# Optimization experiments

Hardware: AMD Instinct MI355X
Metric: run time of the kernel (lower is better)

The kernel has to match this reference:

```python
import jax, jax.numpy as jnp
import numpy as np

B, L, D = 4, 2048, 1024


def setup_inputs() -> dict:
    key = jax.random.key(0)
    ks = jax.random.split(key, 7)
    scale = 1.0 / np.sqrt(D)
    x = jax.random.normal(ks[0], (B, L, D), dtype=jnp.float32)
    wq = jax.random.normal(ks[1], (D, D), dtype=jnp.float32) * scale
    wk = jax.random.normal(ks[2], (D, D), dtype=jnp.float32) * scale
    wv = jax.random.normal(ks[3], (D, D), dtype=jnp.float32) * scale
    bq = jnp.zeros((D,), dtype=jnp.float32)
    bk = jnp.zeros((D,), dtype=jnp.float32)
    bv = jnp.zeros((D,), dtype=jnp.float32)
    # causal decoder mask, shape [B, 1, L, L] as produced by nn.make_causal_mask
    causal = jnp.tril(jnp.ones((L, L), dtype=bool))
    mask = jnp.broadcast_to(causal[None, None, :, :], (B, 1, L, L))
    return {"x": x, "mask": mask, "wq": wq, "bq": bq, "wk": wk, "bk": bk, "wv": wv, "bv": bv}


def reference(x, mask, wq, bq, wk, bk, wv, bv):
    # q/k/v projections (Dense with bias)
    q = x @ wq + bq            # [B, L, D]
    k = x @ wk + bk
    v = x @ wv + bv
    depth = q.shape[-1]
    q = q / jnp.sqrt(jnp.asarray(depth, dtype=q.dtype))
    attn = jnp.einsum('bqd,bkd->bqk', q, k)          # [B, L, L]
    attn = jnp.where(jnp.squeeze(mask), attn, -999999)
    attn = jax.nn.softmax(attn, axis=-1)
    out = attn @ v                                    # [B, L, D]
    return out
```

## Files before the change

kernel.cpp:

```cpp
#include <hip/hip_runtime.h>

typedef __bf16 bf16_t;
typedef __attribute__((ext_vector_type(8))) __bf16 bf16x8;
typedef __attribute__((ext_vector_type(4))) __bf16 bf16x4;
typedef __attribute__((ext_vector_type(4))) float f32x4;

#define B_  4
#define L_  2048
#define D_  1024
#define M_  (B_*L_)
#define N3_ (3*D_)

__device__ __forceinline__ void gload_lds16(const void* g, void* l) {
  __builtin_amdgcn_global_load_lds(
      (__attribute__((address_space(1))) void*)(g),
      (__attribute__((address_space(3))) void*)(l), 16, 0, 0);
}

__device__ __forceinline__ void stage_half(const bf16_t* __restrict__ g, int ld, int grow0,
                                           int k0, bf16_t* lds_tile, int h, int tid) {
  const int lane = tid & 63;
  const int csrc = ((lane & 7) ^ (lane >> 3)) << 3;
  const int rsub = tid >> 3;
  bf16_t* l0 = lds_tile + (size_t)(h * 128 + ((tid >> 6) << 3)) * 64;
  const bf16_t* g0 = g + (size_t)(grow0 + h * 128 + rsub) * ld + (k0 + csrc);
  gload_lds16(g0, l0);
  gload_lds16(g0 + (size_t)64 * ld, l0 + 64 * 64);
}

__global__ __launch_bounds__(512, 2)
void gemm256(const bf16_t* __restrict__ A, int lda,
             const bf16_t* __restrict__ Bt, int ldb,
             bf16_t* __restrict__ C, int ldc,
             const float* __restrict__ b0, const float* __restrict__ b1,
             const float* __restrict__ b2, int K)
{
  const int gx = gridDim.x;
  const int nwg = gx * gridDim.y;
  const int orig = blockIdx.y * gx + blockIdx.x;
  const int swz = (orig & 7) * (nwg >> 3) + (orig >> 3);
  const int bx = swz % gx, by = swz / gx;

  const int r0 = by * 256, c0 = bx * 256;
  const int NT = K >> 6;

  extern __shared__ __align__(16) bf16_t smem[];
  bf16_t* A0 = smem;
  bf16_t* A1 = smem + 16384;
  bf16_t* A2 = smem + 32768;
  bf16_t* B0 = smem + 49152;
  bf16_t* B1 = smem + 65536;

  const int tid = threadIdx.x;
  const int wid = tid >> 6, lane = tid & 63;
  const int wm = wid >> 2, wn = wid & 3;
  const int rl = lane & 15, cg = lane >> 4, x0 = lane & 7;
  const int co0 = ((cg ^ x0) << 3);
  const int co1 = (((4 + cg) ^ x0) << 3);
  const int aoff = (wm * 128 + rl) * 64;
  const int boff = (wn * 64 + rl) * 64;

  f32x4 acc[8][4] = {};
  bf16x8 aLo_[4][2], aHi_[4][2], bF[4][2];

  stage_half(A,  lda, r0, 0,  A0, 0, tid);  stage_half(A,  lda, r0, 0,  A0, 1, tid);
  stage_half(Bt, ldb, c0, 0,  B0, 0, tid);  stage_half(Bt, ldb, c0, 0,  B0, 1, tid);
  stage_half(A,  lda, r0, 64, A1, 0, tid);  stage_half(A,  lda, r0, 64, A1, 1, tid);
  stage_half(Bt, ldb, c0, 64, B1, 0, tid);  stage_half(Bt, ldb, c0, 64, B1, 1, tid);
  asm volatile("s_waitcnt vmcnt(8)" ::: "memory");
  asm volatile("s_barrier" ::: "memory");
  #pragma unroll
  for (int mi = 0; mi < 4; ++mi) {
    aLo_[mi][0] = *(const bf16x8*)(A0 + aoff + mi * 1024 + co0);
    aLo_[mi][1] = *(const bf16x8*)(A0 + aoff + mi * 1024 + co1);
  }

  for (int j = 0; j < NT; ++j) {
    #pragma unroll
    for (int ni = 0; ni < 4; ++ni) {
      bF[ni][0] = *(const bf16x8*)(B0 + boff + ni * 1024 + co0);
      bF[ni][1] = *(const bf16x8*)(B0 + boff + ni * 1024 + co1);
    }
    #pragma unroll
    for (int mi = 0; mi < 4; ++mi) {
      aHi_[mi][0] = *(const bf16x8*)(A0 + aoff + (4 + mi) * 1024 + co0);
      aHi_[mi][1] = *(const bf16x8*)(A0 + aoff + (4 + mi) * 1024 + co1);
    }
    if (j + 2 < NT) {
      stage_half(A, lda, r0, (j + 2) * 64, A2, 0, tid);
      stage_half(A, lda, r0, (j + 2) * 64, A2, 1, tid);
    }
    asm volatile("s_waitcnt lgkmcnt(0)" ::: "memory");
    __builtin_amdgcn_sched_barrier(0);
    __builtin_amdgcn_s_setprio(1);
    #pragma unroll
    for (int mi = 0; mi < 4; ++mi)
      #pragma unroll
      for (int ni = 0; ni < 4; ++ni) {
        acc[mi][ni] = __builtin_amdgcn_mfma_f32_16x16x32_bf16(
            bF[ni][0], aLo_[mi][0], acc[mi][ni], 0, 0, 0);
        acc[mi][ni] = __builtin_amdgcn_mfma_f32_16x16x32_bf16(
            bF[ni][1], aLo_[mi][1], acc[mi][ni], 0, 0, 0);
      }
    __builtin_amdgcn_s_setprio(0);
    if (j + 2 < NT) asm volatile("s_waitcnt vmcnt(4)" ::: "memory");
    else            asm volatile("s_waitcnt vmcnt(0)" ::: "memory");
    asm volatile("s_barrier" ::: "memory");

    if (j + 1 < NT) {
      #pragma unroll
      for (int mi = 0; mi < 4; ++mi) {
        aLo_[mi][0] = *(const bf16x8*)(A1 + aoff + mi * 1024 + co0);
        aLo_[mi][1] = *(const bf16x8*)(A1 + aoff + mi * 1024 + co1);
      }
      if (j + 2 < NT) {
        stage_half(Bt, ldb, c0, (j + 2) * 64, B0, 0, tid);
        stage_half(Bt, ldb, c0, (j + 2) * 64, B0, 1, tid);
      }
      asm volatile("s_waitcnt lgkmcnt(8)" ::: "memory");
    } else {
      asm volatile("s_waitcnt lgkmcnt(0)" ::: "memory");
    }
    __builtin_amdgcn_sched_barrier(0);
    __builtin_amdgcn_s_setprio(1);
    #pragma unroll
    for (int mi = 0; mi < 4; ++mi)
      #pragma unroll
      for (int ni = 0; ni < 4; ++ni) {
        acc[4 + mi][ni] = __builtin_amdgcn_mfma_f32_16x16x32_bf16(
            bF[ni][0], aHi_[mi][0], acc[4 + mi][ni], 0, 0, 0);
        acc[4 + mi][ni] = __builtin_amdgcn_mfma_f32_16x16x32_bf16(
            bF[ni][1], aHi_[mi][1], acc[4 + mi][ni], 0, 0, 0);
      }
    __builtin_amdgcn_s_setprio(0);
    asm volatile("s_barrier" ::: "memory");

    bf16_t* t = A0; A0 = A1; A1 = A2; A2 = t;
    t = B0; B0 = B1; B1 = t;
  }

  const int ng = cg * 4;
  #pragma unroll
  for (int mi = 0; mi < 8; ++mi) {
    const int r = r0 + wm * 128 + mi * 16 + rl;
    #pragma unroll
    for (int ni = 0; ni < 4; ++ni) {
      const int c = c0 + wn * 64 + ni * 16 + ng;
      const float* bias = (c < D_) ? b0 : (c < 2 * D_) ? b1 : b2;
      const float4 bb = *(const float4*)(bias + (c & (D_ - 1)));
      const float sc = (c < D_) ? 0.03125f : 1.0f;
      f32x4 v = acc[mi][ni];
      bf16x4 o = {(bf16_t)((v[0] + bb.x) * sc), (bf16_t)((v[1] + bb.y) * sc),
                  (bf16_t)((v[2] + bb.z) * sc), (bf16_t)((v[3] + bb.w) * sc)};
      *(bf16x4*)(C + (size_t)r * ldc + c) = o;
    }
  }
}

#define KTILE(J, AC, AN1, AN2, BCr, BNx, bC, bN)                                  \
  do {                                                                            \
    const int j_ = (J);                                                           \
    _Pragma("unroll")                                                             \
    for (int mi = 0; mi < 4; ++mi) {                                              \
      aM1_[mi][0] = *(const bf16x8*)(AC + abase + (4 + mi) * 2048 + co0);         \
      aM1_[mi][1] = *(const bf16x8*)(AC + abase + (4 + mi) * 2048 + co1);         \
    }                                                                             \
    if (j_ + 2 < NT) {                                                            \
      stage_half(A, lda, r0, (j_ + 2) * 64, AN2, 0, tid);                         \
      stage_half(A, lda, r0, (j_ + 2) * 64, AN2, 1, tid);                         \
    }                                                                             \
    asm volatile("s_waitcnt lgkmcnt(8)" ::: "memory");                            \
    __builtin_amdgcn_sched_barrier(0);                                            \
    __builtin_amdgcn_s_setprio(1);                                                \
    _Pragma("unroll")                                                             \
    for (int mi = 0; mi < 4; ++mi)                                                \
      _Pragma("unroll")                                                           \
      for (int ni = 0; ni < 2; ++ni) {                                            \
        acc[mi][ni] = __builtin_amdgcn_mfma_f32_16x16x32_bf16(                    \
            bC[ni][0], aM0_[mi][0], acc[mi][ni], 0, 0, 0);                        \
        acc[mi][ni] = __builtin_amdgcn_mfma_f32_16x16x32_bf16(                    \
            bC[ni][1], aM0_[mi][1], acc[mi][ni], 0, 0, 0);                        \
      }                                                                           \
    __builtin_amdgcn_s_setprio(0);                                                \
    if (j_ + 2 < NT) asm volatile("s_waitcnt vmcnt(4)" ::: "memory");             \
    else             asm volatile("s_waitcnt vmcnt(0)" ::: "memory");             \
    asm volatile("s_barrier" ::: "memory");                                       \
    if (j_ + 1 < NT) {                                                            \
      _Pragma("unroll")                                                           \
      for (int mi = 0; mi < 4; ++mi) {                                            \
        aM0_[mi][0] = *(const bf16x8*)(AN1 + abase + mi * 2048 + co0);            \
        aM0_[mi][1] = *(const bf16x8*)(AN1 + abase + mi * 2048 + co1);            \
      }                                                                           \
      _Pragma("unroll")                                                           \
      for (int ni = 0; ni < 2; ++ni) {                                            \
        bN[ni][0] = *(const bf16x8*)(BNx + bbase + ni * 1024 + co0);              \
        bN[ni][1] = *(const bf16x8*)(BNx + bbase + ni * 1024 + co1);              \
      }                                                                           \
      if (j_ + 2 < NT)                                                            \
        stage_half(Bt, ldb, c0, (j_ + 2) * 64, BCr, 0, tid);                      \
      asm volatile("s_waitcnt lgkmcnt(12)" ::: "memory");                         \
    } else {                                                                      \
      asm volatile("s_waitcnt lgkmcnt(0)" ::: "memory");                          \
    }                                                                             \
    __builtin_amdgcn_sched_barrier(0);                                            \
    __builtin_amdgcn_s_setprio(1);                                                \
    _Pragma("unroll")                                                             \
    for (int mi = 0; mi < 4; ++mi)                                                \
      _Pragma("unroll")                                                           \
      for (int ni = 0; ni < 2; ++ni) {                                            \
        acc[4 + mi][ni] = __builtin_amdgcn_mfma_f32_16x16x32_bf16(                \
            bC[ni][0], aM1_[mi][0], acc[4 + mi][ni], 0, 0, 0);                    \
        acc[4 + mi][ni] = __builtin_amdgcn_mfma_f32_16x16x32_bf16(                \
            bC[ni][1], aM1_[mi][1], acc[4 + mi][ni], 0, 0, 0);                    \
      }                                                                           \
    __builtin_amdgcn_s_setprio(0);                                                \
    asm volatile("s_barrier" ::: "memory");                                       \
  } while (0)

template<bool OUT_BF16, bool CAUSAL, bool VARK>
__global__ __launch_bounds__(512, 2)
void gemm8(const bf16_t* __restrict__ A, int lda, long sA,
           const bf16_t* __restrict__ Bt, int ldb, long sB,
           void* __restrict__ Cv, int ldc, long sC, int K)
{
  const int gx = gridDim.x;
  const int nwg = gx * gridDim.y;
  const int orig = blockIdx.y * gx + blockIdx.x;
  const int swz = (orig & 7) * (nwg >> 3) + (orig >> 3);
  const int bx = swz % gx, by = swz / gx;
  if (CAUSAL && bx > 2 * by + 1) return;

  const int z = blockIdx.z;
  A  += (size_t)z * sA;
  Bt += (size_t)z * sB;

  const int r0 = by * 256, c0 = bx * 128;
  const int kend = VARK ? min(K, r0 + 256) : K;
  const int NT = kend >> 6;

  extern __shared__ __align__(16) bf16_t smem[];
  bf16_t* Ab0 = smem;
  bf16_t* Ab1 = smem + 16384;
  bf16_t* Ab2 = smem + 32768;
  bf16_t* Bb0 = smem + 49152;
  bf16_t* Bb1 = smem + 57344;

  const int tid = threadIdx.x;
  const int wid = tid >> 6, lane = tid & 63;
  const int wm = wid >> 2, wn = wid & 3;
  const int rl = lane & 15, cg = lane >> 4, x0 = lane & 7;
  const int co0 = ((cg ^ x0) << 3);
  const int co1 = (((4 + cg) ^ x0) << 3);
  const int abase = (wm * 16 + rl) * 64;
  const int bbase = (wn * 32 + rl) * 64;

  f32x4 acc[8][2] = {};
  bf16x8 aM0_[4][2], aM1_[4][2];
  bf16x8 bA_[2][2], bB_[2][2];

  stage_half(A,  lda, r0, 0,  Ab0, 0, tid);
  stage_half(A,  lda, r0, 0,  Ab0, 1, tid);
  stage_half(Bt, ldb, c0, 0,  Bb0, 0, tid);
  stage_half(A,  lda, r0, 64, Ab1, 0, tid);
  stage_half(A,  lda, r0, 64, Ab1, 1, tid);
  stage_half(Bt, ldb, c0, 64, Bb1, 0, tid);
  asm volatile("s_waitcnt vmcnt(6)" ::: "memory");
  asm volatile("s_barrier" ::: "memory");
  #pragma unroll
  for (int mi = 0; mi < 4; ++mi) {
    aM0_[mi][0] = *(const bf16x8*)(Ab0 + abase + mi * 2048 + co0);
    aM0_[mi][1] = *(const bf16x8*)(Ab0 + abase + mi * 2048 + co1);
  }
  #pragma unroll
  for (int ni = 0; ni < 2; ++ni) {
    bA_[ni][0] = *(const bf16x8*)(Bb0 + bbase + ni * 1024 + co0);
    bA_[ni][1] = *(const bf16x8*)(Bb0 + bbase + ni * 1024 + co1);
  }

  bf16_t *A0 = Ab0, *A1 = Ab1, *A2 = Ab2;
  for (int j = 0; j < NT; j += 2) {
    KTILE(j,     A0, A1, A2, Bb0, Bb1, bA_, bB_);
    KTILE(j + 1, A1, A2, A0, Bb1, Bb0, bB_, bA_);
    bf16_t* t = A2; A2 = A1; A1 = A0; A0 = t;
  }

  const int ml = lane & 15, ng = cg * 4;
  #pragma unroll
  for (int mi = 0; mi < 8; ++mi) {
    const int r = r0 + mi * 32 + wm * 16 + ml;
    #pragma unroll
    for (int ni = 0; ni < 2; ++ni) {
      const int c = c0 + wn * 32 + ni * 16 + ng;
      f32x4 v = acc[mi][ni];
      if (OUT_BF16) {
        bf16x4 o = {(bf16_t)v[0], (bf16_t)v[1], (bf16_t)v[2], (bf16_t)v[3]};
        *(bf16x4*)((bf16_t*)Cv + (size_t)z * sC + (size_t)r * ldc + c) = o;
      } else {
        *(f32x4*)((float*)Cv + (size_t)z * sC + (size_t)r * ldc + c) = v;
      }
    }
  }
}

__device__ __forceinline__ float blk_red_max(float v, float* red, int lane, int wid) {
  #pragma unroll
  for (int o = 32; o; o >>= 1) v = fmaxf(v, __shfl_down(v, o));
  __syncthreads();
  if (lane == 0) red[wid] = v;
  __syncthreads();
  return fmaxf(fmaxf(red[0], red[1]), fmaxf(red[2], red[3]));
}
__device__ __forceinline__ float blk_red_sum(float v, float* red, int lane, int wid) {
  #pragma unroll
  for (int o = 32; o; o >>= 1) v += __shfl_down(v, o);
  __syncthreads();
  if (lane == 0) red[wid] = v;
  __syncthreads();
  return red[0] + red[1] + red[2] + red[3];
}

__global__ __launch_bounds__(256)
void softmax_causal(const bf16_t* __restrict__ S, bf16_t* __restrict__ P) {
  const int r = blockIdx.x;
  const int n = r + 1;
  const int kend = min(((n + 255) >> 8) << 8, L_);
  const bf16_t* row = S + (size_t)blockIdx.y * L_ * L_ + (size_t)r * L_;
  bf16_t* prow = P + (size_t)blockIdx.y * L_ * L_ + (size_t)r * L_;
  const int tid = threadIdx.x, lane = tid & 63, wid = tid >> 6;
  __shared__ float red[4];

  float s[8];
  #pragma unroll
  for (int i = 0; i < 8; ++i) {
    const int c = tid + i * 256;
    s[i] = (c < n) ? (float)row[c] : -3.402823466e38f;
  }
  float mx = -3.402823466e38f;
  #pragma unroll
  for (int i = 0; i < 8; ++i) mx = fmaxf(mx, s[i]);
  mx = blk_red_max(mx, red, lane, wid);

  float e[8]; float sum = 0.f;
  #pragma unroll
  for (int i = 0; i < 8; ++i) {
    const int c = tid + i * 256;
    const float v = (c < n) ? __expf(s[i] - mx) : 0.f;
    e[i] = v; sum += v;
  }
  sum = blk_red_sum(sum, red, lane, wid);
  const float inv = 1.0f / sum;
  #pragma unroll
  for (int i = 0; i < 8; ++i) {
    const int c = tid + i * 256;
    if (c < kend) prow[c] = (bf16_t)(e[i] * inv);
  }
}

__global__ void cvt_f32_bf16(const float* __restrict__ in, bf16_t* __restrict__ out, int n4) {
  const int stride = gridDim.x * blockDim.x;
  for (int i = blockIdx.x * blockDim.x + threadIdx.x; i < n4; i += stride) {
    const float4 v = ((const float4*)in)[i];
    bf16x4 o = { (bf16_t)v.x, (bf16_t)v.y, (bf16_t)v.z, (bf16_t)v.w };
    ((bf16x4*)out)[i] = o;
  }
}

__global__ void transpose_w3(const float* __restrict__ w0, const float* __restrict__ w1,
                             const float* __restrict__ w2, bf16_t* __restrict__ oT) {
  const float* w = blockIdx.z == 0 ? w0 : (blockIdx.z == 1 ? w1 : w2);
  bf16_t* o = oT + (size_t)blockIdx.z * D_ * D_;
  __shared__ float t[32][33];
  const int tx = threadIdx.x, ty = threadIdx.y;
  const int x  = blockIdx.x * 32 + tx;
  const int y0 = blockIdx.y * 32;
  #pragma unroll
  for (int j = 0; j < 4; ++j)
    t[ty + j * 8][tx] = w[(size_t)(y0 + ty + j * 8) * D_ + x];
  __syncthreads();
  const int x2 = y0 + tx;
  const int y2 = blockIdx.x * 32;
  #pragma unroll
  for (int j = 0; j < 4; ++j)
    o[(size_t)(y2 + ty + j * 8) * D_ + x2] = (bf16_t)t[tx][ty + j * 8];
}

__global__ void transpose_bf16(const bf16_t* __restrict__ in, int ld_in, int coff,
                               bf16_t* __restrict__ out, int R, int C) {
  __shared__ bf16_t t[32][34];
  const int tx = threadIdx.x, ty = threadIdx.y;
  const int x  = blockIdx.x * 32 + tx;
  const int y0 = blockIdx.y * 32;
  #pragma unroll
  for (int j = 0; j < 4; ++j)
    t[ty + j * 8][tx] = in[(size_t)(y0 + ty + j * 8) * ld_in + coff + x];
  __syncthreads();
  const int x2 = y0 + tx;
  const int y2 = blockIdx.x * 32;
  #pragma unroll
  for (int j = 0; j < 4; ++j)
    out[(size_t)(y2 + ty + j * 8) * R + x2] = t[tx][ty + j * 8];
}

extern "C" void kernel_launch(void* const* d_in, const int* in_sizes, int n_in,
                              void* d_out, int out_size, void* d_ws, size_t ws_size,
                              hipStream_t stream) {
  const float* x  = (const float*)d_in[0];
  const float* wq = (const float*)d_in[2];
  const float* bq = (const float*)d_in[3];
  const float* wk = (const float*)d_in[4];
  const float* bk = (const float*)d_in[5];
  const float* wv = (const float*)d_in[6];
  const float* bv = (const float*)d_in[7];
  float* out = (float*)d_out;

  bf16_t* xb   = (bf16_t*)d_ws;
  bf16_t* wT   = xb  + (size_t)M_ * D_;
  bf16_t* qkv  = wT  + (size_t)N3_ * D_;
  bf16_t* vbT  = qkv + (size_t)M_ * N3_;
  bf16_t* Sb   = vbT + (size_t)M_ * D_;
  bf16_t* Pfull = qkv;

  const size_t SMEM128 = 131072;
  const size_t SMEM256 = 163840;

  static bool attr_done = false;
  if (!attr_done) {
    hipFuncSetAttribute((const void*)gemm256,
                        hipFuncAttributeMaxDynamicSharedMemorySize, (int)SMEM256);
    hipFuncSetAttribute((const void*)gemm8<true, true, false>,
                        hipFuncAttributeMaxDynamicSharedMemorySize, (int)SMEM128);
    hipFuncSetAttribute((const void*)gemm8<false, false, true>,
                        hipFuncAttributeMaxDynamicSharedMemorySize, (int)SMEM128);
    attr_done = true;
  }

  cvt_f32_bf16<<<1024, 256, 0, stream>>>(x, xb, M_ * D_ / 4);
  transpose_w3<<<dim3(32, 32, 3), dim3(32, 8), 0, stream>>>(wq, wk, wv, wT);

  gemm256<<<dim3(N3_ / 256, M_ / 256), 512, SMEM256, stream>>>(
      xb, D_, wT, D_, qkv, N3_, bq, bk, bv, D_);

  transpose_bf16<<<dim3(D_ / 32, M_ / 32), dim3(32, 8), 0, stream>>>(qkv, N3_, 2 * D_, vbT, M_, D_);

  gemm8<true, true, false><<<dim3(L_ / 128, L_ / 256, B_), 512, SMEM128, stream>>>(
      qkv, N3_, (long)L_ * N3_, qkv + D_, N3_, (long)L_ * N3_, Sb, L_, (long)L_ * L_, D_);

  softmax_causal<<<dim3(L_, B_), 256, 0, stream>>>(Sb, Pfull);

  gemm8<false, false, true><<<dim3(D_ / 128, L_ / 256, B_), 512, SMEM128, stream>>>(
      Pfull, L_, (long)L_ * L_, vbT, M_, (long)L_, out, D_, (long)L_ * D_, L_);
}
```

Baseline: 189.2 us.

## Generalize 256x256 GEMM with batching and causal skip; use it for QK^T scores

```diff
diff --git a/kernel.cpp b/kernel.cpp
--- a/kernel.cpp
+++ b/kernel.cpp
@@ -28,28 +28,29 @@
   gload_lds16(g0 + (size_t)64 * ld, l0 + 64 * 64);
 }
 
+template<bool OUT_BF16, bool CAUSAL, bool PROJ>
 __global__ __launch_bounds__(512, 2)
-void gemm256(const bf16_t* __restrict__ A, int lda,
-             const bf16_t* __restrict__ Bt, int ldb,
-             bf16_t* __restrict__ C, int ldc,
-             const float* __restrict__ b0, const float* __restrict__ b1,
-             const float* __restrict__ b2, int K)
+void gemm256ks(const bf16_t* __restrict__ A, int lda, long sA,
+               const bf16_t* __restrict__ Bt, int ldb, long sB,
+               void* __restrict__ Cv, int ldc, long sC,
+               const float* __restrict__ b0, const float* __restrict__ b1,
+               const float* __restrict__ b2, int K)
 {
   const int gx = gridDim.x;
   const int nwg = gx * gridDim.y;
   const int orig = blockIdx.y * gx + blockIdx.x;
   const int swz = (orig & 7) * (nwg >> 3) + (orig >> 3);
   const int bx = swz % gx, by = swz / gx;
+  if (CAUSAL && bx > by) return;
+
+  const int z = blockIdx.z;
+  A  += (size_t)z * sA;
+  Bt += (size_t)z * sB;
 
   const int r0 = by * 256, c0 = bx * 256;
   const int NT = K >> 6;
 
   extern __shared__ __align__(16) bf16_t smem[];
-  bf16_t* A0 = smem;
-  bf16_t* A1 = smem + 16384;
-  bf16_t* A2 = smem + 32768;
-  bf16_t* B0 = smem + 49152;
-  bf16_t* B1 = smem + 65536;
 
   const int tid = threadIdx.x;
   const int wid = tid >> 6, lane = tid & 63;
@@ -61,47 +62,53 @@
   const int boff = (wn * 64 + rl) * 64;
 
   f32x4 acc[8][4] = {};
-  bf16x8 aLo_[4][2], aHi_[4][2], bF[4][2];
-
-  stage_half(A,  lda, r0, 0,  A0, 0, tid);  stage_half(A,  lda, r0, 0,  A0, 1, tid);
-  stage_half(Bt, ldb, c0, 0,  B0, 0, tid);  stage_half(Bt, ldb, c0, 0,  B0, 1, tid);
-  stage_half(A,  lda, r0, 64, A1, 0, tid);  stage_half(A,  lda, r0, 64, A1, 1, tid);
-  stage_half(Bt, ldb, c0, 64, B1, 0, tid);  stage_half(Bt, ldb, c0, 64, B1, 1, tid);
-  asm volatile("s_waitcnt vmcnt(8)" ::: "memory");
+  bf16x8 aP[8], aQ[8], bP[4], bQ[4];
+
+  stage_half(A,  lda, r0, 0,  smem,         0, tid);
+  stage_half(A,  lda, r0, 0,  smem,         1, tid);
+  stage_half(Bt, ldb, c0, 0,  smem + 49152, 0, tid);
+  stage_half(Bt, ldb, c0, 0,  smem + 49152, 1, tid);
+  stage_half(A,  lda, r0, 64, smem + 16384, 0, tid);
+  stage_half(A,  lda, r0, 64, smem + 16384, 1, tid);
+  asm volatile("s_waitcnt vmcnt(4)" ::: "memory");
   asm volatile("s_barrier" ::: "memory");
   #pragma unroll
-  for (int mi = 0; mi < 4; ++mi) {
-    aLo_[mi][0] = *(const bf16x8*)(A0 + aoff + mi * 1024 + co0);
-    aLo_[mi][1] = *(const bf16x8*)(A0 + aoff + mi * 1024 + co1);
-  }
+  for (int mi = 0; mi < 8; ++mi)
+    aP[mi] = *(const bf16x8*)(smem + aoff + mi * 1024 + co0);
+  #pragma unroll
+  for (int ni = 0; ni < 4; ++ni)
+    bP[ni] = *(const bf16x8*)(smem + 49152 + boff + ni * 1024 + co0);
 
   for (int j = 0; j < NT; ++j) {
-    #pragma unroll
-    for (int ni = 0; ni < 4; ++ni) {
-      bF[ni][0] = *(const bf16x8*)(B0 + boff + ni * 1024 + co0);
-      bF[ni][1] = *(const bf16x8*)(B0 + boff + ni * 1024 + co1);
-    }
-    #pragma unroll
-    for (int mi = 0; mi < 4; ++mi) {
-      aHi_[mi][0] = *(const bf16x8*)(A0 + aoff + (4 + mi) * 1024 + co0);
-      aHi_[mi][1] = *(const bf16x8*)(A0 + aoff + (4 + mi) * 1024 + co1);
+    bf16_t* Acur = smem + (j % 3) * 16384;
+    bf16_t* Bcur = smem + 49152 + (j & 1) * 16384;
+    bf16_t* Anxt = smem + ((j + 1) % 3) * 16384;
+    bf16_t* Bnxt = smem + 49152 + ((j + 1) & 1) * 16384;
+    bf16_t* Anx2 = smem + ((j + 2) % 3) * 16384;
+
+    #pragma unroll
+    for (int mi = 0; mi < 8; ++mi)
+      aQ[mi] = *(const bf16x8*)(Acur + aoff + mi * 1024 + co1);
+    #pragma unroll
+    for (int ni = 0; ni < 4; ++ni)
+      bQ[ni] = *(const bf16x8*)(Bcur + boff + ni * 1024 + co1);
+    if (j + 1 < NT) {
+      stage_half(Bt, ldb, c0, (j + 1) * 64, Bnxt, 0, tid);
+      stage_half(Bt, ldb, c0, (j + 1) * 64, Bnxt, 1, tid);
     }
     if (j + 2 < NT) {
-      stage_half(A, lda, r0, (j + 2) * 64, A2, 0, tid);
-      stage_half(A, lda, r0, (j + 2) * 64, A2, 1, tid);
+      stage_half(A, lda, r0, (j + 2) * 64, Anx2, 0, tid);
+      stage_half(A, lda, r0, (j + 2) * 64, Anx2, 1, tid);
     }
-    asm volatile("s_waitcnt lgkmcnt(0)" ::: "memory");
+    asm volatile("s_waitcnt lgkmcnt(12)" ::: "memory");
     __builtin_amdgcn_sched_barrier(0);
     __builtin_amdgcn_s_setprio(1);
     #pragma unroll
-    for (int mi = 0; mi < 4; ++mi)
+    for (int mi = 0; mi < 8; ++mi)
       #pragma unroll
-      for (int ni = 0; ni < 4; ++ni) {
+      for (int ni = 0; ni < 4; ++ni)
         acc[mi][ni] = __builtin_amdgcn_mfma_f32_16x16x32_bf16(
-            bF[ni][0], aLo_[mi][0], acc[mi][ni], 0, 0, 0);
-        acc[mi][ni] = __builtin_amdgcn_mfma_f32_16x16x32_bf16(
-            bF[ni][1], aLo_[mi][1], acc[mi][ni], 0, 0, 0);
-      }
+            bP[ni], aP[mi], acc[mi][ni], 0, 0, 0);
     __builtin_amdgcn_s_setprio(0);
     if (j + 2 < NT) asm volatile("s_waitcnt vmcnt(4)" ::: "memory");
     else            asm volatile("s_waitcnt vmcnt(0)" ::: "memory");
@@ -109,34 +116,25 @@
 
     if (j + 1 < NT) {
       #pragma unroll
-      for (int mi = 0; mi < 4; ++mi) {
-        aLo_[mi][0] = *(const bf16x8*)(A1 + aoff + mi * 1024 + co0);
-        aLo_[mi][1] = *(const bf16x8*)(A1 + aoff + mi * 1024 + co1);
-      }
-      if (j + 2 < NT) {
-        stage_half(Bt, ldb, c0, (j + 2) * 64, B0, 0, tid);
-        stage_half(Bt, ldb, c0, (j + 2) * 64, B0, 1, tid);
-      }
-      asm volatile("s_waitcnt lgkmcnt(8)" ::: "memory");
+      for (int mi = 0; mi < 8; ++mi)
+        aP[mi] = *(const bf16x8*)(Anxt + aoff + mi * 1024 + co0);
+      #pragma unroll
+      for (int ni = 0; ni < 4; ++ni)
+        bP[ni] = *(const bf16x8*)(Bnxt + boff + ni * 1024 + co0);
+      asm volatile("s_waitcnt lgkmcnt(12)" ::: "memory");
     } else {
       asm volatile("s_waitcnt lgkmcnt(0)" ::: "memory");
     }
     __builtin_amdgcn_sched_barrier(0);
     __builtin_amdgcn_s_setprio(1);
     #pragma unroll
-    for (int mi = 0; mi < 4; ++mi)
+    for (int mi = 0; mi < 8; ++mi)
       #pragma unroll
-      for (int ni = 0; ni < 4; ++ni) {
-        acc[4 + mi][ni] = __builtin_amdgcn_mfma_f32_16x16x32_bf16(
-            bF[ni][0], aHi_[mi][0], acc[4 + mi][ni], 0, 0, 0);
-        acc[4 + mi][ni] = __builtin_amdgcn_mfma_f32_16x16x32_bf16(
-            bF[ni][1], aHi_[mi][1], acc[4 + mi][ni], 0, 0, 0);
-      }
+      for (int ni = 0; ni < 4; ++ni)
+        acc[mi][ni] = __builtin_amdgcn_mfma_f32_16x16x32_bf16(
+            bQ[ni], aQ[mi], acc[mi][ni], 0, 0, 0);
     __builtin_amdgcn_s_setprio(0);
     asm volatile("s_barrier" ::: "memory");
-
-    bf16_t* t = A0; A0 = A1; A1 = A2; A2 = t;
-    t = B0; B0 = B1; B1 = t;
   }
 
   const int ng = cg * 4;
@@ -146,13 +144,20 @@
     #pragma unroll
     for (int ni = 0; ni < 4; ++ni) {
       const int c = c0 + wn * 64 + ni * 16 + ng;
-      const float* bias = (c < D_) ? b0 : (c < 2 * D_) ? b1 : b2;
-      const float4 bb = *(const float4*)(bias + (c & (D_ - 1)));
-      const float sc = (c < D_) ? 0.03125f : 1.0f;
       f32x4 v = acc[mi][ni];
-      bf16x4 o = {(bf16_t)((v[0] + bb.x) * sc), (bf16_t)((v[1] + bb.y) * sc),
-                  (bf16_t)((v[2] + bb.z) * sc), (bf16_t)((v[3] + bb.w) * sc)};
-      *(bf16x4*)(C + (size_t)r * ldc + c) = o;
+      if (PROJ) {
+        const float* bias = (c < D_) ? b0 : (c < 2 * D_) ? b1 : b2;
+        const float4 bb = *(const float4*)(bias + (c & (D_ - 1)));
+        const float sc = (c < D_) ? 0.03125f : 1.0f;
+        v[0] = (v[0] + bb.x) * sc; v[1] = (v[1] + bb.y) * sc;
+        v[2] = (v[2] + bb.z) * sc; v[3] = (v[3] + bb.w) * sc;
+      }
+      if (OUT_BF16) {
+        bf16x4 o = {(bf16_t)v[0], (bf16_t)v[1], (bf16_t)v[2], (bf16_t)v[3]};
+        *(bf16x4*)((bf16_t*)Cv + (size_t)z * sC + (size_t)r * ldc + c) = o;
+      } else {
+        *(f32x4*)((float*)Cv + (size_t)z * sC + (size_t)r * ldc + c) = v;
+      }
     }
   }
 }
@@ -421,29 +426,26 @@
   bf16_t* Pfull = qkv;
 
   const size_t SMEM128 = 131072;
-  const size_t SMEM256 = 163840;
-
-  static bool attr_done = false;
-  if (!attr_done) {
-    hipFuncSetAttribute((const void*)gemm256,
-                        hipFuncAttributeMaxDynamicSharedMemorySize, (int)SMEM256);
-    hipFuncSetAttribute((const void*)gemm8<true, true, false>,
-                        hipFuncAttributeMaxDynamicSharedMemorySize, (int)SMEM128);
-    hipFuncSetAttribute((const void*)gemm8<false, false, true>,
-                        hipFuncAttributeMaxDynamicSharedMemorySize, (int)SMEM128);
-    attr_done = true;
-  }
+  const size_t SMEM160 = 163840;
+
+  (void)hipFuncSetAttribute((const void*)gemm256ks<true, false, true>,
+                      hipFuncAttributeMaxDynamicSharedMemorySize, (int)SMEM160);
+  (void)hipFuncSetAttribute((const void*)gemm256ks<true, true, false>,
+                      hipFuncAttributeMaxDynamicSharedMemorySize, (int)SMEM160);
+  (void)hipFuncSetAttribute((const void*)gemm8<false, false, true>,
+                      hipFuncAttributeMaxDynamicSharedMemorySize, (int)SMEM128);
 
   cvt_f32_bf16<<<1024, 256, 0, stream>>>(x, xb, M_ * D_ / 4);
   transpose_w3<<<dim3(32, 32, 3), dim3(32, 8), 0, stream>>>(wq, wk, wv, wT);
 
-  gemm256<<<dim3(N3_ / 256, M_ / 256), 512, SMEM256, stream>>>(
-      xb, D_, wT, D_, qkv, N3_, bq, bk, bv, D_);
+  gemm256ks<true, false, true><<<dim3(N3_ / 256, M_ / 256), 512, SMEM160, stream>>>(
+      xb, D_, 0, wT, D_, 0, qkv, N3_, 0, bq, bk, bv, D_);
 
   transpose_bf16<<<dim3(D_ / 32, M_ / 32), dim3(32, 8), 0, stream>>>(qkv, N3_, 2 * D_, vbT, M_, D_);
 
-  gemm8<true, true, false><<<dim3(L_ / 128, L_ / 256, B_), 512, SMEM128, stream>>>(
-      qkv, N3_, (long)L_ * N3_, qkv + D_, N3_, (long)L_ * N3_, Sb, L_, (long)L_ * L_, D_);
+  gemm256ks<true, true, false><<<dim3(L_ / 256, L_ / 256, B_), 512, SMEM160, stream>>>(
+      qkv, N3_, (long)L_ * N3_, qkv + D_, N3_, (long)L_ * N3_, Sb, L_, (long)L_ * L_,
+      nullptr, nullptr, nullptr, D_);
 
   softmax_causal<<<dim3(L_, B_), 256, 0, stream>>>(Sb, Pfull);
 
```

Result: no change. 192.5 us (+1.7%).
